# Kernel optimization log

Hardware: AMD Instinct MI355X
Metric: run time of the kernel (lower is better)

The kernel has to match this reference:

```python
import jax, jax.numpy as jnp
import numpy as np

N_VOX = 200000
Z, Y, X = 41, 256, 256


def _build_rulebook(N, seed=0):
    """Build submanifold 3x3x3 rulebook: nbr[i,k] = voxel index of neighbor k of voxel i, or -1."""
    rng = np.random.default_rng(seed)
    keys = np.unique(rng.integers(0, Z * Y * X, size=int(N * 1.3)))
    assert keys.shape[0] >= N
    keys = keys[:N]  # sorted unique linearized coords
    z = keys // (Y * X)
    rem = keys % (Y * X)
    y = rem // X
    x = rem % X
    nbr = np.full((N, 27), -1, np.int32)
    k = 0
    for dz in (-1, 0, 1):
        for dy in (-1, 0, 1):
            for dx in (-1, 0, 1):
                nz, ny, nx = z + dz, y + dy, x + dx
                valid = (nz >= 0) & (nz < Z) & (ny >= 0) & (ny < Y) & (nx >= 0) & (nx < X)
                nkey = (nz * Y + ny) * X + nx
                pos = np.searchsorted(keys, nkey)
                pos_c = np.minimum(pos, N - 1)
                found = valid & (keys[pos_c] == nkey)
                nbr[:, k] = np.where(found, pos_c, -1)
                k += 1
    return nbr


def setup_inputs() -> dict:
    key = jax.random.key(0)
    ks = jax.random.split(key, 8)
    nbr = jnp.asarray(_build_rulebook(N_VOX))
    return {
        "voxel_features": jax.random.normal(ks[0], (N_VOX, 4), jnp.float32),
        "nbr_idx": nbr,
        "W0": jax.random.normal(ks[1], (27, 4, 16), jnp.float32) * 0.05,
        "s0": jnp.ones((16,), jnp.float32),
        "b0": jnp.zeros((16,), jnp.float32),
        "W1": jax.random.normal(ks[2], (27, 16, 16), jnp.float32) * 0.05,
        "s1": jnp.ones((16,), jnp.float32),
        "b1": jnp.zeros((16,), jnp.float32),
        "W2": jax.random.normal(ks[3], (27, 16, 16), jnp.float32) * 0.05,
        "s2": jnp.ones((16,), jnp.float32),
        "b2": jnp.zeros((16,), jnp.float32),
        "W_lin": jax.random.normal(ks[4], (16, 3), jnp.float32) * 0.05,
        "b_lin": jnp.zeros((3,), jnp.float32),
    }


def _subm_conv(feats, W, nbr, mask):
    # feats: [N, Cin], W: [27, Cin, Cout], nbr: [N, 27] (rulebook), mask: [N, 27, 1]
    g = jnp.take(feats, jnp.maximum(nbr, 0), axis=0) * mask  # [N, 27, Cin] gather (memory-bound)
    return jnp.einsum("nkc,kcd->nd", g, W)  # scatter-free dense contraction


def reference(voxel_features, nbr_idx, W0, s0, b0, W1, s1, b1, W2, s2, b2, W_lin, b_lin):
    mask = (nbr_idx >= 0)[..., None].astype(voxel_features.dtype)
    # conv_input: SubMConv3d(4,16,3) + BN(folded to scale/shift) + ReLU
    x = jax.nn.relu(_subm_conv(voxel_features, W0, nbr_idx, mask) * s0 + b0)
    # SparseBasicBlock(16,16, indice_key='subm1'): conv-bn-relu-conv-bn + residual + relu
    idn = x
    h = jax.nn.relu(_subm_conv(x, W1, nbr_idx, mask) * s1 + b1)
    h = _subm_conv(h, W2, nbr_idx, mask) * s2 + b2
    x = jax.nn.relu(h + idn)
    # mos_seg_layer: Linear(16, mos_class)
    return x @ W_lin + b_lin
```

## Files before the change

### kernel.cpp

```cpp
#include <hip/hip_runtime.h>

#define NVOX 200000

__device__ __forceinline__ void fma16x16(const float4* __restrict__ wrow,
                                         float4 f0, float4 f1, float4 f2, float4 f3,
                                         float acc[16]) {
    const float g[16] = {f0.x, f0.y, f0.z, f0.w, f1.x, f1.y, f1.z, f1.w,
                         f2.x, f2.y, f2.z, f2.w, f3.x, f3.y, f3.z, f3.w};
    #pragma unroll
    for (int cc = 0; cc < 16; ++cc) {
        float gc = g[cc];
        float4 w0 = wrow[cc * 4 + 0];
        float4 w1 = wrow[cc * 4 + 1];
        float4 w2 = wrow[cc * 4 + 2];
        float4 w3 = wrow[cc * 4 + 3];
        acc[0]  += gc * w0.x; acc[1]  += gc * w0.y; acc[2]  += gc * w0.z; acc[3]  += gc * w0.w;
        acc[4]  += gc * w1.x; acc[5]  += gc * w1.y; acc[6]  += gc * w1.z; acc[7]  += gc * w1.w;
        acc[8]  += gc * w2.x; acc[9]  += gc * w2.y; acc[10] += gc * w2.z; acc[11] += gc * w2.w;
        acc[12] += gc * w3.x; acc[13] += gc * w3.y; acc[14] += gc * w3.z; acc[15] += gc * w3.w;
    }
}

__global__ __launch_bounds__(256) void k1_compact_conv0(
    const float* __restrict__ feats,
    const int* __restrict__ nbr,
    const float* __restrict__ W,
    const float* __restrict__ s, const float* __restrict__ b,
    int* __restrict__ ent,
    int* __restrict__ cnt,
    float* __restrict__ x) {
    __shared__ int   lnbr[256 * 27];
    __shared__ float Wl[27 * 68];
    int t = threadIdx.x;
    int base = blockIdx.x * 256;
    for (int i = t; i < 27 * 64; i += 256)
        Wl[(i >> 6) * 68 + (i & 63)] = W[i];
    int nv = NVOX - base; if (nv > 256) nv = 256;
    int count = nv * 27;
    const int* gsrc = nbr + base * 27;
    for (int i = t; i < count; i += 256)
        lnbr[i] = gsrc[i];
    __syncthreads();

    int n = base + t;
    if (n >= NVOX) return;
    int* row = lnbr + t * 27;
    int c = 0;
    #pragma unroll
    for (int k = 0; k < 27; ++k) {
        int idx = row[k];
        if (idx >= 0) {
            int e = (idx << 5) | k;
            row[c] = e;
            ent[c * NVOX + n] = e;
            ++c;
        }
    }
    cnt[n] = c;

    float acc[16];
    #pragma unroll
    for (int d = 0; d < 16; ++d) acc[d] = 0.f;
    int e = row[0];
    float4 f = *(const float4*)(feats + (e >> 5) * 4);
    int j = 0;
    while (true) {
        bool more = (++j < c);
        int en = e; float4 fn = f;
        if (more) {
            en = row[j];
            fn = *(const float4*)(feats + (en >> 5) * 4);
        }
        {
            const float4* wrow = (const float4*)(Wl + (e & 31) * 68);
            float g[4] = {f.x, f.y, f.z, f.w};
            #pragma unroll
            for (int cc = 0; cc < 4; ++cc) {
                float gc = g[cc];
                float4 w0 = wrow[cc * 4 + 0];
                float4 w1 = wrow[cc * 4 + 1];
                float4 w2 = wrow[cc * 4 + 2];
                float4 w3 = wrow[cc * 4 + 3];
                acc[0]  += gc * w0.x; acc[1]  += gc * w0.y; acc[2]  += gc * w0.z; acc[3]  += gc * w0.w;
                acc[4]  += gc * w1.x; acc[5]  += gc * w1.y; acc[6]  += gc * w1.z; acc[7]  += gc * w1.w;
                acc[8]  += gc * w2.x; acc[9]  += gc * w2.y; acc[10] += gc * w2.z; acc[11] += gc * w2.w;
                acc[12] += gc * w3.x; acc[13] += gc * w3.y; acc[14] += gc * w3.z; acc[15] += gc * w3.w;
            }
        }
        if (!more) break;
        e = en; f = fn;
    }
    float4* o = (float4*)(x + n * 16);
    #pragma unroll
    for (int q = 0; q < 4; ++q) {
        float4 r;
        float v0 = acc[q * 4 + 0] * s[q * 4 + 0] + b[q * 4 + 0];
        float v1 = acc[q * 4 + 1] * s[q * 4 + 1] + b[q * 4 + 1];
        float v2 = acc[q * 4 + 2] * s[q * 4 + 2] + b[q * 4 + 2];
        float v3 = acc[q * 4 + 3] * s[q * 4 + 3] + b[q * 4 + 3];
        r.x = v0 > 0.f ? v0 : 0.f;
        r.y = v1 > 0.f ? v1 : 0.f;
        r.z = v2 > 0.f ? v2 : 0.f;
        r.w = v3 > 0.f ? v3 : 0.f;
        o[q] = r;
    }
}

__device__ __forceinline__ void conv16_core(const float* __restrict__ fin,
                                            const int* __restrict__ ent,
                                            int c, int n, const float* Wl,
                                            float acc[16]) {
    int e = ent[n];
    const float4* fp = (const float4*)(fin + (e >> 5) * 16);
    float4 f0 = fp[0], f1 = fp[1], f2 = fp[2], f3 = fp[3];
    int j = 0;
    while (true) {
        bool more = (++j < c);
        int en = e;
        float4 g0 = f0, g1 = f1, g2 = f2, g3 = f3;
        if (more) {
            en = ent[j * NVOX + n];
            const float4* fq = (const float4*)(fin + (en >> 5) * 16);
            g0 = fq[0]; g1 = fq[1]; g2 = fq[2]; g3 = fq[3];
        }
        fma16x16((const float4*)(Wl + (e & 31) * 260), f0, f1, f2, f3, acc);
        if (!more) break;
        e = en; f0 = g0; f1 = g1; f2 = g2; f3 = g3;
    }
}

__global__ __launch_bounds__(256) void k2_conv1(
    const float* __restrict__ fin,
    const int* __restrict__ ent, const int* __restrict__ cnt,
    const float* __restrict__ W,
    const float* __restrict__ s, const float* __restrict__ b,
    float* __restrict__ out) {
    __shared__ float Wl[27 * 260];
    for (int i = threadIdx.x; i < 27 * 256; i += 256)
        Wl[(i >> 8) * 260 + (i & 255)] = W[i];
    __syncthreads();
    int n = blockIdx.x * 256 + threadIdx.x;
    if (n >= NVOX) return;
    int c = cnt[n];
    float acc[16];
    #pragma unroll
    for (int d = 0; d < 16; ++d) acc[d] = 0.f;
    conv16_core(fin, ent, c, n, Wl, acc);
    float4* o = (float4*)(out + n * 16);
    #pragma unroll
    for (int q = 0; q < 4; ++q) {
        float4 r;
        float v0 = acc[q * 4 + 0] * s[q * 4 + 0] + b[q * 4 + 0];
        float v1 = acc[q * 4 + 1] * s[q * 4 + 1] + b[q * 4 + 1];
        float v2 = acc[q * 4 + 2] * s[q * 4 + 2] + b[q * 4 + 2];
        float v3 = acc[q * 4 + 3] * s[q * 4 + 3] + b[q * 4 + 3];
        r.x = v0 > 0.f ? v0 : 0.f;
        r.y = v1 > 0.f ? v1 : 0.f;
        r.z = v2 > 0.f ? v2 : 0.f;
        r.w = v3 > 0.f ? v3 : 0.f;
        o[q] = r;
    }
}

__global__ __launch_bounds__(256) void k3_conv2_final(
    const float* __restrict__ fin,
    const int* __restrict__ ent, const int* __restrict__ cnt,
    const float* __restrict__ W,
    const float* __restrict__ s, const float* __restrict__ b,
    const float* __restrict__ idn,
    const float* __restrict__ Wlin,
    const float* __restrict__ blin,
    float* __restrict__ out) {
    __shared__ float Wl[27 * 260];
    for (int i = threadIdx.x; i < 27 * 256; i += 256)
        Wl[(i >> 8) * 260 + (i & 255)] = W[i];
    __syncthreads();
    int n = blockIdx.x * 256 + threadIdx.x;
    if (n >= NVOX) return;
    int c = cnt[n];
    float acc[16];
    #pragma unroll
    for (int d = 0; d < 16; ++d) acc[d] = 0.f;
    conv16_core(fin, ent, c, n, Wl, acc);
    const float4* ip = (const float4*)(idn + n * 16);
    float4 i0 = ip[0], i1 = ip[1], i2 = ip[2], i3 = ip[3];
    float id[16] = {i0.x, i0.y, i0.z, i0.w, i1.x, i1.y, i1.z, i1.w,
                    i2.x, i2.y, i2.z, i2.w, i3.x, i3.y, i3.z, i3.w};
    float o0 = blin[0], o1 = blin[1], o2 = blin[2];
    #pragma unroll
    for (int d = 0; d < 16; ++d) {
        float v = acc[d] * s[d] + b[d] + id[d];
        v = v > 0.f ? v : 0.f;
        o0 += v * Wlin[d * 3 + 0];
        o1 += v * Wlin[d * 3 + 1];
        o2 += v * Wlin[d * 3 + 2];
    }
    out[n * 3 + 0] = o0;
    out[n * 3 + 1] = o1;
    out[n * 3 + 2] = o2;
}

extern "C" void kernel_launch(void* const* d_in, const int* in_sizes, int n_in,
                              void* d_out, int out_size, void* d_ws, size_t ws_size,
                              hipStream_t stream) {
    const float* feats = (const float*)d_in[0];
    const int*   nbr   = (const int*)d_in[1];
    const float* W0    = (const float*)d_in[2];
    const float* s0    = (const float*)d_in[3];
    const float* b0    = (const float*)d_in[4];
    const float* W1    = (const float*)d_in[5];
    const float* s1    = (const float*)d_in[6];
    const float* b1    = (const float*)d_in[7];
    const float* W2    = (const float*)d_in[8];
    const float* s2    = (const float*)d_in[9];
    const float* b2    = (const float*)d_in[10];
    const float* Wlin  = (const float*)d_in[11];
    const float* blin  = (const float*)d_in[12];
    float* out = (float*)d_out;

    char* ws = (char*)d_ws;
    int*   ent = (int*)(ws);
    int*   cnt = (int*)(ws + 21600000);
    float* x   = (float*)(ws + 22400000);
    float* h   = (float*)(ws + 35200000);

    int blocks = (NVOX + 255) / 256;
    k1_compact_conv0<<<blocks, 256, 0, stream>>>(feats, nbr, W0, s0, b0, ent, cnt, x);
    k2_conv1<<<blocks, 256, 0, stream>>>(x, ent, cnt, W1, s1, b1, h);
    k3_conv2_final<<<blocks, 256, 0, stream>>>(h, ent, cnt, W2, s2, b2, x, Wlin, blin, out);
}
```

Before: 67.66 us.

## Switch conv1/conv2 to per-tile edge-parallel entries with LDS atomic accumulation

```diff
diff --git a/kernel.cpp b/kernel.cpp
--- a/kernel.cpp
+++ b/kernel.cpp
@@ -1,6 +1,9 @@
 #include <hip/hip_runtime.h>
 
 #define NVOX 200000
+#define TILE 256
+#define ETILE 1024
+#define NTILES ((NVOX + TILE - 1) / TILE)
 
 __device__ __forceinline__ void fma16x16(const float4* __restrict__ wrow,
                                          float4 f0, float4 f1, float4 f2, float4 f3,
@@ -26,38 +29,65 @@
     const int* __restrict__ nbr,
     const float* __restrict__ W,
     const float* __restrict__ s, const float* __restrict__ b,
-    int* __restrict__ ent,
-    int* __restrict__ cnt,
+    int* __restrict__ gEnt,
+    int* __restrict__ tileCnt,
     float* __restrict__ x) {
-    __shared__ int   lnbr[256 * 27];
+    __shared__ int   lnbr[TILE * 27];
     __shared__ float Wl[27 * 68];
+    __shared__ int   khist[27];
+    __shared__ int   kbase[28];
+    __shared__ int   eloc[ETILE];
     int t = threadIdx.x;
-    int base = blockIdx.x * 256;
+    int tile = blockIdx.x;
+    int base = tile * TILE;
     for (int i = t; i < 27 * 64; i += 256)
         Wl[(i >> 6) * 68 + (i & 63)] = W[i];
-    int nv = NVOX - base; if (nv > 256) nv = 256;
-    int count = nv * 27;
+    if (t < 27) khist[t] = 0;
+    int nv = NVOX - base; if (nv > TILE) nv = TILE;
     const int* gsrc = nbr + base * 27;
-    for (int i = t; i < count; i += 256)
+    for (int i = t; i < nv * 27; i += 256)
         lnbr[i] = gsrc[i];
     __syncthreads();
 
-    int n = base + t;
-    if (n >= NVOX) return;
+    int c = 0;
     int* row = lnbr + t * 27;
-    int c = 0;
-    #pragma unroll
-    for (int k = 0; k < 27; ++k) {
-        int idx = row[k];
-        if (idx >= 0) {
-            int e = (idx << 5) | k;
-            row[c] = e;
-            ent[c * NVOX + n] = e;
-            ++c;
-        }
-    }
-    cnt[n] = c;
-
+    if (t < nv) {
+        #pragma unroll
+        for (int k = 0; k < 27; ++k) {
+            int idx = row[k];
+            if (idx >= 0) {
+                row[c] = (idx << 5) | k;
+                atomicAdd(&khist[k], 1);
+                ++c;
+            }
+        }
+    }
+    __syncthreads();
+    if (t == 0) {
+        int a = 0;
+        for (int k = 0; k < 27; ++k) { kbase[k] = a; a += khist[k]; }
+        kbase[27] = a;
+        tileCnt[tile] = a < ETILE ? a : ETILE;
+    }
+    __syncthreads();
+    if (t < 27) khist[t] = 0;
+    __syncthreads();
+    if (t < nv) {
+        for (int j = 0; j < c; ++j) {
+            int e = row[j];
+            int k = e & 31;
+            int idx = e >> 5;
+            int pos = kbase[k] + atomicAdd(&khist[k], 1);
+            if (pos < ETILE)
+                eloc[pos] = (idx << 14) | (k << 9) | t;
+        }
+    }
+    __syncthreads();
+    int tot = kbase[27] < ETILE ? kbase[27] : ETILE;
+    for (int i = t; i < tot; i += 256)
+        gEnt[tile * ETILE + i] = eloc[i];
+
+    if (t >= nv) return;
     float acc[16];
     #pragma unroll
     for (int d = 0; d < 16; ++d) acc[d] = 0.f;
@@ -90,6 +120,7 @@
         if (!more) break;
         e = en; f = fn;
     }
+    int n = base + t;
     float4* o = (float4*)(x + n * 16);
     #pragma unroll
     for (int q = 0; q < 4; ++q) {
@@ -106,54 +137,66 @@
     }
 }
 
-__device__ __forceinline__ void conv16_core(const float* __restrict__ fin,
-                                            const int* __restrict__ ent,
-                                            int c, int n, const float* Wl,
-                                            float acc[16]) {
-    int e = ent[n];
-    const float4* fp = (const float4*)(fin + (e >> 5) * 16);
+__device__ __forceinline__ void conv_tile_accum(const float* __restrict__ fin,
+                                                const int* __restrict__ ep, int cntE,
+                                                const float* __restrict__ Wl,
+                                                float* __restrict__ ot, int t) {
+    int i = t;
+    if (i >= cntE) return;
+    unsigned e = (unsigned)ep[i];
+    const float4* fp = (const float4*)(fin + (e >> 14) * 16);
     float4 f0 = fp[0], f1 = fp[1], f2 = fp[2], f3 = fp[3];
-    int j = 0;
     while (true) {
-        bool more = (++j < c);
-        int en = e;
+        int i2 = i + 256;
+        bool more = (i2 < cntE);
+        unsigned e2 = e;
         float4 g0 = f0, g1 = f1, g2 = f2, g3 = f3;
         if (more) {
-            en = ent[j * NVOX + n];
-            const float4* fq = (const float4*)(fin + (en >> 5) * 16);
+            e2 = (unsigned)ep[i2];
+            const float4* fq = (const float4*)(fin + (e2 >> 14) * 16);
             g0 = fq[0]; g1 = fq[1]; g2 = fq[2]; g3 = fq[3];
         }
-        fma16x16((const float4*)(Wl + (e & 31) * 260), f0, f1, f2, f3, acc);
+        int k  = (e >> 9) & 31;
+        int nl = e & 511;
+        float acc[16];
+        #pragma unroll
+        for (int d = 0; d < 16; ++d) acc[d] = 0.f;
+        fma16x16((const float4*)(Wl + k * 256), f0, f1, f2, f3, acc);
+        float* orow = ot + nl * 17;
+        #pragma unroll
+        for (int d = 0; d < 16; ++d)
+            atomicAdd(&orow[d], acc[d]);
         if (!more) break;
-        e = en; f0 = g0; f1 = g1; f2 = g2; f3 = g3;
+        i = i2; e = e2; f0 = g0; f1 = g1; f2 = g2; f3 = g3;
     }
 }
 
 __global__ __launch_bounds__(256) void k2_conv1(
     const float* __restrict__ fin,
-    const int* __restrict__ ent, const int* __restrict__ cnt,
+    const int* __restrict__ gEnt, const int* __restrict__ tileCnt,
     const float* __restrict__ W,
     const float* __restrict__ s, const float* __restrict__ b,
     float* __restrict__ out) {
-    __shared__ float Wl[27 * 260];
-    for (int i = threadIdx.x; i < 27 * 256; i += 256)
-        Wl[(i >> 8) * 260 + (i & 255)] = W[i];
-    __syncthreads();
-    int n = blockIdx.x * 256 + threadIdx.x;
+    __shared__ float Wl[27 * 256];
+    __shared__ float ot[TILE * 17];
+    int t = threadIdx.x;
+    int tile = blockIdx.x;
+    for (int i = t; i < 27 * 256; i += 256) Wl[i] = W[i];
+    for (int i = t; i < TILE * 17; i += 256) ot[i] = 0.f;
+    __syncthreads();
+    conv_tile_accum(fin, gEnt + tile * ETILE, tileCnt[tile], Wl, ot, t);
+    __syncthreads();
+    int n = tile * TILE + t;
     if (n >= NVOX) return;
-    int c = cnt[n];
-    float acc[16];
-    #pragma unroll
-    for (int d = 0; d < 16; ++d) acc[d] = 0.f;
-    conv16_core(fin, ent, c, n, Wl, acc);
+    const float* orow = ot + t * 17;
     float4* o = (float4*)(out + n * 16);
     #pragma unroll
     for (int q = 0; q < 4; ++q) {
         float4 r;
-        float v0 = acc[q * 4 + 0] * s[q * 4 + 0] + b[q * 4 + 0];
-        float v1 = acc[q * 4 + 1] * s[q * 4 + 1] + b[q * 4 + 1];
-        float v2 = acc[q * 4 + 2] * s[q * 4 + 2] + b[q * 4 + 2];
-        float v3 = acc[q * 4 + 3] * s[q * 4 + 3] + b[q * 4 + 3];
+        float v0 = orow[q * 4 + 0] * s[q * 4 + 0] + b[q * 4 + 0];
+        float v1 = orow[q * 4 + 1] * s[q * 4 + 1] + b[q * 4 + 1];
+        float v2 = orow[q * 4 + 2] * s[q * 4 + 2] + b[q * 4 + 2];
+        float v3 = orow[q * 4 + 3] * s[q * 4 + 3] + b[q * 4 + 3];
         r.x = v0 > 0.f ? v0 : 0.f;
         r.y = v1 > 0.f ? v1 : 0.f;
         r.z = v2 > 0.f ? v2 : 0.f;
@@ -164,24 +207,25 @@
 
 __global__ __launch_bounds__(256) void k3_conv2_final(
     const float* __restrict__ fin,
-    const int* __restrict__ ent, const int* __restrict__ cnt,
+    const int* __restrict__ gEnt, const int* __restrict__ tileCnt,
     const float* __restrict__ W,
     const float* __restrict__ s, const float* __restrict__ b,
     const float* __restrict__ idn,
     const float* __restrict__ Wlin,
     const float* __restrict__ blin,
     float* __restrict__ out) {
-    __shared__ float Wl[27 * 260];
-    for (int i = threadIdx.x; i < 27 * 256; i += 256)
-        Wl[(i >> 8) * 260 + (i & 255)] = W[i];
-    __syncthreads();
-    int n = blockIdx.x * 256 + threadIdx.x;
+    __shared__ float Wl[27 * 256];
+    __shared__ float ot[TILE * 17];
+    int t = threadIdx.x;
+    int tile = blockIdx.x;
+    for (int i = t; i < 27 * 256; i += 256) Wl[i] = W[i];
+    for (int i = t; i < TILE * 17; i += 256) ot[i] = 0.f;
+    __syncthreads();
+    conv_tile_accum(fin, gEnt + tile * ETILE, tileCnt[tile], Wl, ot, t);
+    __syncthreads();
+    int n = tile * TILE + t;
     if (n >= NVOX) return;
-    int c = cnt[n];
-    float acc[16];
-    #pragma unroll
-    for (int d = 0; d < 16; ++d) acc[d] = 0.f;
-    conv16_core(fin, ent, c, n, Wl, acc);
+    const float* orow = ot + t * 17;
     const float4* ip = (const float4*)(idn + n * 16);
     float4 i0 = ip[0], i1 = ip[1], i2 = ip[2], i3 = ip[3];
     float id[16] = {i0.x, i0.y, i0.z, i0.w, i1.x, i1.y, i1.z, i1.w,
@@ -189,7 +233,7 @@
     float o0 = blin[0], o1 = blin[1], o2 = blin[2];
     #pragma unroll
     for (int d = 0; d < 16; ++d) {
-        float v = acc[d] * s[d] + b[d] + id[d];
+        float v = orow[d] * s[d] + b[d] + id[d];
         v = v > 0.f ? v : 0.f;
         o0 += v * Wlin[d * 3 + 0];
         o1 += v * Wlin[d * 3 + 1];
@@ -219,13 +263,12 @@
     float* out = (float*)d_out;
 
     char* ws = (char*)d_ws;
-    int*   ent = (int*)(ws);
-    int*   cnt = (int*)(ws + 21600000);
-    float* x   = (float*)(ws + 22400000);
-    float* h   = (float*)(ws + 35200000);
-
-    int blocks = (NVOX + 255) / 256;
-    k1_compact_conv0<<<blocks, 256, 0, stream>>>(feats, nbr, W0, s0, b0, ent, cnt, x);
-    k2_conv1<<<blocks, 256, 0, stream>>>(x, ent, cnt, W1, s1, b1, h);
-    k3_conv2_final<<<blocks, 256, 0, stream>>>(h, ent, cnt, W2, s2, b2, x, Wlin, blin, out);
-}
+    int*   gEnt    = (int*)(ws);
+    int*   tileCnt = (int*)(ws + 3203072);
+    float* x       = (float*)(ws + 3208192);
+    float* h       = (float*)(ws + 16008192);
+
+    k1_compact_conv0<<<NTILES, 256, 0, stream>>>(feats, nbr, W0, s0, b0, gEnt, tileCnt, x);
+    k2_conv1<<<NTILES, 256, 0, stream>>>(x, gEnt, tileCnt, W1, s1, b1, h);
+    k3_conv2_final<<<NTILES, 256, 0, stream>>>(h, gEnt, tileCnt, W2, s2, b2, x, Wlin, blin, out);
+}
```

Result: slower. 185.4 us (+174.1%).
